# Kernel optimization log

Measured on AMD Instinct MI355X. Metric: run time of the kernel, lower is better.

## Reference

```python
import jax, jax.numpy as jnp
import numpy as np

B, S, D, CH = 2048, 16, 512, 1024


def setup_inputs() -> dict:
    key = jax.random.key(0)
    ks = jax.random.split(key, 12)
    sc = lambda fan: 1.0 / np.sqrt(fan)
    return {
        "local_descs_t": jax.random.normal(ks[0], (B, S, D), jnp.float32),
        "local_descs_rot": jax.random.normal(ks[1], (B, S, D), jnp.float32),
        "w_scene": jax.random.normal(ks[2], (2 * D,), jnp.float32) * sc(2 * D),
        "b_scene": jnp.zeros((1,), jnp.float32),
        "Wh_t": jax.random.normal(ks[3], (S, D, CH), jnp.float32) * sc(D),
        "bh_t": jnp.zeros((S, CH), jnp.float32),
        "Wo_t": jax.random.normal(ks[4], (S, CH, 3), jnp.float32) * sc(CH),
        "bo_t": jnp.zeros((S, 3), jnp.float32),
        "Wh_r": jax.random.normal(ks[5], (S, D, CH), jnp.float32) * sc(D),
        "bh_r": jnp.zeros((S, CH), jnp.float32),
        "Wo_r": jax.random.normal(ks[6], (S, CH, 4), jnp.float32) * sc(CH),
        "bo_r": jnp.zeros((S, 4), jnp.float32),
    }


def _expert_head(x, onehot, Wh, bh, Wo, bo):
    # x: [B, D] gathered global descriptor; run all S experts, combine by one-hot
    h = jax.nn.gelu(jnp.einsum("bd,sdh->bsh", x, Wh) + bh, approximate=False)
    o = jnp.einsum("bsh,sho->bso", h, Wo) + bo  # [B, S, out]
    return jnp.einsum("bs,bso->bo", onehot, o)


def reference(local_descs_t, local_descs_rot, w_scene, b_scene,
              Wh_t, bh_t, Wo_t, bo_t, Wh_r, bh_r, Wo_r, bo_r):
    # scene router: Linear(2D -> 1) over concatenated descriptors, log_softmax over scenes
    cat = jnp.concatenate([local_descs_t, local_descs_rot], axis=2)  # [B, S, 2D]
    logits = jnp.einsum("bsd,d->bs", cat, w_scene) + b_scene[0]
    scene_log_distr = jax.nn.log_softmax(logits, axis=1)  # [B, S]
    max_indices = jnp.argmax(scene_log_distr, axis=1)  # [B]
    onehot = jax.nn.one_hot(max_indices, S, dtype=local_descs_t.dtype)
    # combine: gather selected scene's descriptor (torch code uses dense mask w)
    global_desc_t = jnp.einsum("bs,bsd->bd", onehot, local_descs_t)
    global_desc_rot = jnp.einsum("bs,bsd->bd", onehot, local_descs_rot)
    # per-sample expert heads (Linear -> GELU -> Linear)
    x_t = _expert_head(global_desc_t, onehot, Wh_t, bh_t, Wo_t, bo_t)    # [B, 3]
    x_rot = _expert_head(global_desc_rot, onehot, Wh_r, bh_r, Wo_r, bo_r)  # [B, 4]
    pose = jnp.concatenate([x_t, x_rot], axis=1)  # [B, 7]
    return pose, scene_log_distr
```

## Files before the change

### kernel.cpp

```cpp
#include <hip/hip_runtime.h>
#include <hip/hip_bf16.h>
#include <math.h>

constexpr int B_  = 2048;
constexpr int S_  = 16;
constexpr int D_  = 512;
constexpr int CH_ = 1024;

constexpr int BM = 64;
constexpr int BN = 128;
constexpr int BK = 64;

typedef __attribute__((ext_vector_type(8))) short bf16x8;
typedef __attribute__((ext_vector_type(4))) float f32x4;

constexpr size_t CNT_OFF  = 0;
constexpr size_t LIST_OFF = 256;

static __device__ __forceinline__ short f2bf(float x) {
    __hip_bfloat16 h = __float2bfloat16(x);
    return *(short*)&h;
}

static __device__ __forceinline__ float gelu_exact(float x) {
    return 0.5f * x * (1.f + erff(x * 0.70710678118654752f));
}

__global__ __launch_bounds__(1024) void k_router_sm(
    const float* __restrict__ ldt, const float* __restrict__ ldr,
    const float* __restrict__ w,   const float* __restrict__ bsc,
    float* __restrict__ sld,
    int* __restrict__ count, int* __restrict__ list)
{
    const int b    = blockIdx.x;
    const int wave = threadIdx.x >> 6;
    const int lane = threadIdx.x & 63;

    __shared__ float lgs[S_];

    const float4* pt = (const float4*)(ldt + ((size_t)b * S_ + wave) * D_);
    const float4* pr = (const float4*)(ldr + ((size_t)b * S_ + wave) * D_);
    const float4* wt = (const float4*)(w);
    const float4* wr = (const float4*)(w + D_);

    float acc = 0.f;
    #pragma unroll
    for (int it = 0; it < 2; it++) {
        const int i = lane + it * 64;
        float4 a  = pt[i]; float4 ww = wt[i];
        acc += a.x * ww.x + a.y * ww.y + a.z * ww.z + a.w * ww.w;
        float4 c  = pr[i]; float4 w2 = wr[i];
        acc += c.x * w2.x + c.y * w2.y + c.z * w2.z + c.w * w2.w;
    }
    #pragma unroll
    for (int off = 32; off > 0; off >>= 1) acc += __shfl_down(acc, off, 64);
    if (lane == 0) lgs[wave] = acc;
    __syncthreads();

    if (threadIdx.x < S_) {
        const int s = threadIdx.x;
        const float v = lgs[s] + bsc[0];
        float mv = v; int mi = s;
        #pragma unroll
        for (int d = 1; d < 16; d <<= 1) {
            float ov = __shfl_xor(mv, d, 16);
            int   oi = __shfl_xor(mi, d, 16);
            if (ov > mv || (ov == mv && oi < mi)) { mv = ov; mi = oi; }
        }
        float e = expf(v - mv);
        float sum = e;
        #pragma unroll
        for (int d = 1; d < 16; d <<= 1) sum += __shfl_xor(sum, d, 16);
        const float lse = mv + logf(sum);
        sld[b * S_ + s] = v - lse;
        if (s == 0) {
            const int pos = atomicAdd(&count[mi], 1);
            list[mi * B_ + pos] = b;
        }
    }
}

__global__ __launch_bounds__(256) void k_expert_mfma(
    const float* __restrict__ ldt, const float* __restrict__ ldr,
    const float* __restrict__ Wht, const float* __restrict__ bht,
    const float* __restrict__ Wot, const float* __restrict__ bot,
    const float* __restrict__ Whr, const float* __restrict__ bhr,
    const float* __restrict__ Wor, const float* __restrict__ bor,
    const int* __restrict__ count, const int* __restrict__ list,
    float* __restrict__ pose)
{
    const int bid  = blockIdx.x;
    const int m    = bid & 15;
    const int head = (bid >> 4) & 1;
    const int ct   = (bid >> 5) & 7;
    const int st   = bid >> 8;

    const int n = count[m];
    if (st * BM >= n) return;

    const float* __restrict__ xsrc = head ? ldr : ldt;
    const float* __restrict__ Wh   = head ? Whr : Wht;
    const float* __restrict__ bh   = head ? bhr : bht;
    const float* __restrict__ Wo   = head ? Wor : Wot;
    const float* __restrict__ bo   = head ? bor : bot;
    const int noj    = head ? 4 : 3;
    const int jobase = head ? 3 : 0;

    const int ch0 = ct * BN;

    __shared__ short As[BM * BK];
    __shared__ short Bs[BN * BK];
    __shared__ int   bidx[BM];

    const int tid  = threadIdx.x;
    const int wave = tid >> 6;
    const int lane = tid & 63;
    const int wr   = wave >> 1;
    const int wc   = wave & 1;
    const int rbase = wr * 32;
    const int cbase = wc * 64;

    if (tid < BM) {
        const int gi = st * BM + tid;
        bidx[tid] = (gi < n) ? list[m * B_ + gi] : -1;
    }
    __syncthreads();

    f32x4 acc[2][4] = {};

    for (int k0 = 0; k0 < D_; k0 += BK) {
        {
            const int r  = tid >> 2;
            const int kc = (tid & 3) * 16;
            const int bb = bidx[r];
            float4 v0, v1, v2, v3;
            if (bb >= 0) {
                const float4* src = (const float4*)(xsrc + ((size_t)bb * S_ + m) * D_ + k0 + kc);
                v0 = src[0]; v1 = src[1]; v2 = src[2]; v3 = src[3];
            } else {
                v0 = v1 = v2 = v3 = make_float4(0.f, 0.f, 0.f, 0.f);
            }
            short tmp[16];
            tmp[0]=f2bf(v0.x); tmp[1]=f2bf(v0.y); tmp[2]=f2bf(v0.z); tmp[3]=f2bf(v0.w);
            tmp[4]=f2bf(v1.x); tmp[5]=f2bf(v1.y); tmp[6]=f2bf(v1.z); tmp[7]=f2bf(v1.w);
            tmp[8]=f2bf(v2.x); tmp[9]=f2bf(v2.y); tmp[10]=f2bf(v2.z); tmp[11]=f2bf(v2.w);
            tmp[12]=f2bf(v3.x); tmp[13]=f2bf(v3.y); tmp[14]=f2bf(v3.z); tmp[15]=f2bf(v3.w);
            const int u0 = kc >> 3;
            *(bf16x8*)&As[r * 64 + ((u0     ^ (r & 7)) << 3)] = *(bf16x8*)&tmp[0];
            *(bf16x8*)&As[r * 64 + (((u0+1) ^ (r & 7)) << 3)] = *(bf16x8*)&tmp[8];
        }
        {
            const int k  = tid >> 2;
            const size_t rowbase = (size_t)m * D_ * CH_ + (size_t)(k0 + k) * CH_ + ch0;
            #pragma unroll
            for (int i = 0; i < 8; i++) {
                const int chl = (tid & 3) * 4 + i * 16;
                const float4 wv = *(const float4*)(Wh + rowbase + chl);
                #pragma unroll
                for (int c = 0; c < 4; c++) {
                    const int ch = chl + c;
                    const float f = (c == 0) ? wv.x : (c == 1) ? wv.y : (c == 2) ? wv.z : wv.w;
                    Bs[ch * 64 + (((k >> 3) ^ (ch & 7)) << 3) + (k & 7)] = f2bf(f);
                }
            }
        }
        __syncthreads();

        #pragma unroll
        for (int kk = 0; kk < BK; kk += 32) {
            const int ub = (kk >> 3) + (lane >> 4);
            bf16x8 a[2], bfr[4];
            #pragma unroll
            for (int fm = 0; fm < 2; fm++) {
                const int r = rbase + fm * 16 + (lane & 15);
                a[fm] = *(bf16x8*)&As[r * 64 + ((ub ^ (r & 7)) << 3)];
            }
            #pragma unroll
            for (int fn = 0; fn < 4; fn++) {
                const int c = cbase + fn * 16 + (lane & 15);
                bfr[fn] = *(bf16x8*)&Bs[c * 64 + ((ub ^ (c & 7)) << 3)];
            }
            #pragma unroll
            for (int fm = 0; fm < 2; fm++)
                #pragma unroll
                for (int fn = 0; fn < 4; fn++)
                    acc[fm][fn] = __builtin_amdgcn_mfma_f32_16x16x32_bf16(a[fm], bfr[fn], acc[fm][fn], 0, 0, 0);
        }
        __syncthreads();
    }

    float g[2][4][4];
    float wo_l[4][4];
    #pragma unroll
    for (int fn = 0; fn < 4; fn++) {
        const int ch = ch0 + cbase + fn * 16 + (lane & 15);
        const float bias = bh[m * CH_ + ch];
        #pragma unroll
        for (int fm = 0; fm < 2; fm++)
            #pragma unroll
            for (int j = 0; j < 4; j++)
                g[fm][fn][j] = gelu_exact(acc[fm][fn][j] + bias);
        #pragma unroll
        for (int jo = 0; jo < 4; jo++)
            wo_l[fn][jo] = (jo < noj) ? Wo[(size_t)(m * CH_ + ch) * noj + jo] : 0.f;
    }

    #pragma unroll
    for (int fm = 0; fm < 2; fm++) {
        #pragma unroll
        for (int j = 0; j < 4; j++) {
            const int lr = rbase + fm * 16 + ((lane >> 4) << 2) + j;
            const int bb = bidx[lr];
            #pragma unroll
            for (int jo = 0; jo < 4; jo++) {
                if (jo >= noj) continue;
                float v = 0.f;
                #pragma unroll
                for (int fn = 0; fn < 4; fn++) v += g[fm][fn][j] * wo_l[fn][jo];
                #pragma unroll
                for (int d = 1; d < 16; d <<= 1) v += __shfl_xor(v, d, 16);
                if ((lane & 15) == 0 && bb >= 0) {
                    if (ct == 0 && wc == 0) v += bo[m * noj + jo];
                    atomicAdd(&pose[(size_t)bb * 7 + jobase + jo], v);
                }
            }
        }
    }
}

extern "C" void kernel_launch(void* const* d_in, const int* in_sizes, int n_in,
                              void* d_out, int out_size, void* d_ws, size_t ws_size,
                              hipStream_t stream)
{
    const float* ldt = (const float*)d_in[0];
    const float* ldr = (const float*)d_in[1];
    const float* wsc = (const float*)d_in[2];
    const float* bsc = (const float*)d_in[3];
    const float* Wht = (const float*)d_in[4];
    const float* bht = (const float*)d_in[5];
    const float* Wot = (const float*)d_in[6];
    const float* bot = (const float*)d_in[7];
    const float* Whr = (const float*)d_in[8];
    const float* bhr = (const float*)d_in[9];
    const float* Wor = (const float*)d_in[10];
    const float* bor = (const float*)d_in[11];

    float* pose = (float*)d_out;
    float* sld  = (float*)d_out + (size_t)B_ * 7;

    int* count = (int*)((char*)d_ws + CNT_OFF);
    int* list  = (int*)((char*)d_ws + LIST_OFF);

    hipMemsetAsync(count, 0, 16 * sizeof(int), stream);
    hipMemsetAsync(pose, 0, (size_t)B_ * 7 * sizeof(float), stream);

    k_router_sm<<<dim3(B_), dim3(1024), 0, stream>>>(ldt, ldr, wsc, bsc, sld, count, list);

    k_expert_mfma<<<dim3(16 * 2 * 8 * 32), dim3(256), 0, stream>>>(
        ldt, ldr, Wht, bht, Wot, bot, Whr, bhr, Wor, bor, count, list, pose);
}
```

Measured before the change: 83.11 us.

## Software-pipeline expert GEMM with register prefetch and reshaped tiles

Tiles of the expert GEMM change from BN=128,BK=64 to BN=64,BK=128, with padded LDS strides in place of the XOR swizzle. The K loop is fully unrolled with double-buffered register prefetch, so the global loads for the next tile are in flight during the MFMA work on the current one. The block index order is changed so blocks that share an expert's weights and channel tile run close together. The weight load now reads column-strided scalars, which may hurt coalescing, and the grid doubles, which adds more atomic adds per output.

Result: slower. 107.3 us (+29.1%).

```diff
diff --git a/kernel.cpp b/kernel.cpp
--- a/kernel.cpp
+++ b/kernel.cpp
@@ -8,8 +8,10 @@
 constexpr int CH_ = 1024;
 
 constexpr int BM = 64;
-constexpr int BN = 128;
-constexpr int BK = 64;
+constexpr int BN = 64;
+constexpr int BK = 128;
+constexpr int SA = 136;
+constexpr int SB = 136;
 
 typedef __attribute__((ext_vector_type(8))) short bf16x8;
 typedef __attribute__((ext_vector_type(4))) float f32x4;
@@ -21,7 +23,6 @@
     __hip_bfloat16 h = __float2bfloat16(x);
     return *(short*)&h;
 }
-
 static __device__ __forceinline__ float gelu_exact(float x) {
     return 0.5f * x * (1.f + erff(x * 0.70710678118654752f));
 }
@@ -29,8 +30,7 @@
 __global__ __launch_bounds__(1024) void k_router_sm(
     const float* __restrict__ ldt, const float* __restrict__ ldr,
     const float* __restrict__ w,   const float* __restrict__ bsc,
-    float* __restrict__ sld,
-    int* __restrict__ count, int* __restrict__ list)
+    float* __restrict__ sld, int* __restrict__ count, int* __restrict__ list)
 {
     const int b    = blockIdx.x;
     const int wave = threadIdx.x >> 6;
@@ -67,8 +67,7 @@
             int   oi = __shfl_xor(mi, d, 16);
             if (ov > mv || (ov == mv && oi < mi)) { mv = ov; mi = oi; }
         }
-        float e = expf(v - mv);
-        float sum = e;
+        float sum = expf(v - mv);
         #pragma unroll
         for (int d = 1; d < 16; d <<= 1) sum += __shfl_xor(sum, d, 16);
         const float lse = mv + logf(sum);
@@ -90,10 +89,10 @@
     float* __restrict__ pose)
 {
     const int bid  = blockIdx.x;
-    const int m    = bid & 15;
-    const int head = (bid >> 4) & 1;
-    const int ct   = (bid >> 5) & 7;
-    const int st   = bid >> 8;
+    const int ct   = bid & 15;
+    const int st   = (bid >> 4) & 31;
+    const int head = (bid >> 9) & 1;
+    const int m    = bid >> 10;
 
     const int n = count[m];
     if (st * BM >= n) return;
@@ -105,11 +104,10 @@
     const float* __restrict__ bo   = head ? bor : bot;
     const int noj    = head ? 4 : 3;
     const int jobase = head ? 3 : 0;
-
-    const int ch0 = ct * BN;
-
-    __shared__ short As[BM * BK];
-    __shared__ short Bs[BN * BK];
+    const int ch0    = ct * BN;
+
+    __shared__ short As[BM * SA];
+    __shared__ short Bs[BN * SB];
     __shared__ int   bidx[BM];
 
     const int tid  = threadIdx.x;
@@ -118,7 +116,7 @@
     const int wr   = wave >> 1;
     const int wc   = wave & 1;
     const int rbase = wr * 32;
-    const int cbase = wc * 64;
+    const int cbase = wc * 32;
 
     if (tid < BM) {
         const int gi = st * BM + tid;
@@ -126,73 +124,97 @@
     }
     __syncthreads();
 
-    f32x4 acc[2][4] = {};
-
-    for (int k0 = 0; k0 < D_; k0 += BK) {
-        {
-            const int r  = tid >> 2;
-            const int kc = (tid & 3) * 16;
-            const int bb = bidx[r];
-            float4 v0, v1, v2, v3;
-            if (bb >= 0) {
-                const float4* src = (const float4*)(xsrc + ((size_t)bb * S_ + m) * D_ + k0 + kc);
-                v0 = src[0]; v1 = src[1]; v2 = src[2]; v3 = src[3];
-            } else {
-                v0 = v1 = v2 = v3 = make_float4(0.f, 0.f, 0.f, 0.f);
-            }
-            short tmp[16];
+    const int rA = tid >> 2;
+    const int kq = tid & 3;
+    const int bb = bidx[rA];
+    const float* xrow = (bb >= 0) ? (xsrc + ((size_t)bb * S_ + m) * D_) : nullptr;
+
+    const int u2  = tid >> 5;
+    const int chb = tid & 31;
+    const float* wcol = Wh + (size_t)m * D_ * CH_ + ch0 + chb;
+
+    auto loadA = [&](float4* pa, int t) {
+        if (bb >= 0) {
+            const float4* p = (const float4*)(xrow + t * BK) + kq * 8;
+            #pragma unroll
+            for (int i = 0; i < 8; i++) pa[i] = p[i];
+        } else {
+            #pragma unroll
+            for (int i = 0; i < 8; i++) pa[i] = make_float4(0.f, 0.f, 0.f, 0.f);
+        }
+    };
+    auto loadB = [&](float* pb, int t) {
+        #pragma unroll
+        for (int i = 0; i < 4; i++) {
+            const int uu = u2 * 2 + (i >> 1);
+            const float* p = wcol + (size_t)(t * BK + uu * 8) * CH_ + (i & 1) * 32;
+            #pragma unroll
+            for (int j = 0; j < 8; j++) pb[i * 8 + j] = p[(size_t)j * CH_];
+        }
+    };
+    auto storeTiles = [&](const float4* pa, const float* pb) {
+        #pragma unroll
+        for (int c = 0; c < 4; c++) {
+            short tmp[8];
+            const float4 v0 = pa[c * 2], v1 = pa[c * 2 + 1];
             tmp[0]=f2bf(v0.x); tmp[1]=f2bf(v0.y); tmp[2]=f2bf(v0.z); tmp[3]=f2bf(v0.w);
             tmp[4]=f2bf(v1.x); tmp[5]=f2bf(v1.y); tmp[6]=f2bf(v1.z); tmp[7]=f2bf(v1.w);
-            tmp[8]=f2bf(v2.x); tmp[9]=f2bf(v2.y); tmp[10]=f2bf(v2.z); tmp[11]=f2bf(v2.w);
-            tmp[12]=f2bf(v3.x); tmp[13]=f2bf(v3.y); tmp[14]=f2bf(v3.z); tmp[15]=f2bf(v3.w);
-            const int u0 = kc >> 3;
-            *(bf16x8*)&As[r * 64 + ((u0     ^ (r & 7)) << 3)] = *(bf16x8*)&tmp[0];
-            *(bf16x8*)&As[r * 64 + (((u0+1) ^ (r & 7)) << 3)] = *(bf16x8*)&tmp[8];
-        }
-        {
-            const int k  = tid >> 2;
-            const size_t rowbase = (size_t)m * D_ * CH_ + (size_t)(k0 + k) * CH_ + ch0;
-            #pragma unroll
-            for (int i = 0; i < 8; i++) {
-                const int chl = (tid & 3) * 4 + i * 16;
-                const float4 wv = *(const float4*)(Wh + rowbase + chl);
-                #pragma unroll
-                for (int c = 0; c < 4; c++) {
-                    const int ch = chl + c;
-                    const float f = (c == 0) ? wv.x : (c == 1) ? wv.y : (c == 2) ? wv.z : wv.w;
-                    Bs[ch * 64 + (((k >> 3) ^ (ch & 7)) << 3) + (k & 7)] = f2bf(f);
-                }
-            }
-        }
-        __syncthreads();
-
-        #pragma unroll
-        for (int kk = 0; kk < BK; kk += 32) {
-            const int ub = (kk >> 3) + (lane >> 4);
-            bf16x8 a[2], bfr[4];
-            #pragma unroll
-            for (int fm = 0; fm < 2; fm++) {
-                const int r = rbase + fm * 16 + (lane & 15);
-                a[fm] = *(bf16x8*)&As[r * 64 + ((ub ^ (r & 7)) << 3)];
-            }
-            #pragma unroll
-            for (int fn = 0; fn < 4; fn++) {
-                const int c = cbase + fn * 16 + (lane & 15);
-                bfr[fn] = *(bf16x8*)&Bs[c * 64 + ((ub ^ (c & 7)) << 3)];
-            }
+            *(bf16x8*)&As[rA * SA + kq * 32 + c * 8] = *(bf16x8*)tmp;
+        }
+        #pragma unroll
+        for (int i = 0; i < 4; i++) {
+            const int uu = u2 * 2 + (i >> 1);
+            const int ch = chb + (i & 1) * 32;
+            short tmp[8];
+            #pragma unroll
+            for (int j = 0; j < 8; j++) tmp[j] = f2bf(pb[i * 8 + j]);
+            *(bf16x8*)&Bs[ch * SB + uu * 8] = *(bf16x8*)tmp;
+        }
+    };
+
+    f32x4 acc[2][2] = {};
+    auto mfmaTile = [&]() {
+        #pragma unroll
+        for (int kk = 0; kk < 4; kk++) {
+            const int ub = kk * 4 + (lane >> 4);
+            bf16x8 af[2], bfv[2];
+            #pragma unroll
+            for (int fm = 0; fm < 2; fm++)
+                af[fm] = *(bf16x8*)&As[(rbase + fm * 16 + (lane & 15)) * SA + ub * 8];
+            #pragma unroll
+            for (int fn = 0; fn < 2; fn++)
+                bfv[fn] = *(bf16x8*)&Bs[(cbase + fn * 16 + (lane & 15)) * SB + ub * 8];
             #pragma unroll
             for (int fm = 0; fm < 2; fm++)
                 #pragma unroll
-                for (int fn = 0; fn < 4; fn++)
-                    acc[fm][fn] = __builtin_amdgcn_mfma_f32_16x16x32_bf16(a[fm], bfr[fn], acc[fm][fn], 0, 0, 0);
-        }
-        __syncthreads();
-    }
-
-    float g[2][4][4];
-    float wo_l[4][4];
-    #pragma unroll
-    for (int fn = 0; fn < 4; fn++) {
+                for (int fn = 0; fn < 2; fn++)
+                    acc[fm][fn] = __builtin_amdgcn_mfma_f32_16x16x32_bf16(af[fm], bfv[fn], acc[fm][fn], 0, 0, 0);
+        }
+    };
+
+    float4 pa[8], qa[8];
+    float  pb[32], qb[32];
+    loadA(pa, 0); loadB(pb, 0);
+
+    storeTiles(pa, pb); __syncthreads();
+    loadA(qa, 1); loadB(qb, 1);
+    mfmaTile(); __syncthreads();
+
+    storeTiles(qa, qb); __syncthreads();
+    loadA(pa, 2); loadB(pb, 2);
+    mfmaTile(); __syncthreads();
+
+    storeTiles(pa, pb); __syncthreads();
+    loadA(qa, 3); loadB(qb, 3);
+    mfmaTile(); __syncthreads();
+
+    storeTiles(qa, qb); __syncthreads();
+    mfmaTile(); __syncthreads();
+
+    float g[2][2][4];
+    float wo_l[2][4];
+    #pragma unroll
+    for (int fn = 0; fn < 2; fn++) {
         const int ch = ch0 + cbase + fn * 16 + (lane & 15);
         const float bias = bh[m * CH_ + ch];
         #pragma unroll
@@ -210,18 +232,16 @@
         #pragma unroll
         for (int j = 0; j < 4; j++) {
             const int lr = rbase + fm * 16 + ((lane >> 4) << 2) + j;
-            const int bb = bidx[lr];
+            const int bb2 = bidx[lr];
             #pragma unroll
             for (int jo = 0; jo < 4; jo++) {
                 if (jo >= noj) continue;
-                float v = 0.f;
-                #pragma unroll
-                for (int fn = 0; fn < 4; fn++) v += g[fm][fn][j] * wo_l[fn][jo];
+                float v = g[fm][0][j] * wo_l[0][jo] + g[fm][1][j] * wo_l[1][jo];
                 #pragma unroll
                 for (int d = 1; d < 16; d <<= 1) v += __shfl_xor(v, d, 16);
-                if ((lane & 15) == 0 && bb >= 0) {
+                if ((lane & 15) == 0 && bb2 >= 0) {
                     if (ct == 0 && wc == 0) v += bo[m * noj + jo];
-                    atomicAdd(&pose[(size_t)bb * 7 + jobase + jo], v);
+                    atomicAdd(&pose[(size_t)bb2 * 7 + jobase + jo], v);
                 }
             }
         }
@@ -256,6 +276,6 @@
 
     k_router_sm<<<dim3(B_), dim3(1024), 0, stream>>>(ldt, ldr, wsc, bsc, sld, count, list);
 
-    k_expert_mfma<<<dim3(16 * 2 * 8 * 32), dim3(256), 0, stream>>>(
+    k_expert_mfma<<<dim3(16 * 2 * 32 * 16), dim3(256), 0, stream>>>(
         ldt, ldr, Wht, bht, Wot, bot, Whr, bhr, Wor, bor, count, list, pose);
 }
```

## Pre-gather bf16 descriptors in router and use compact tile list without LDS

Applied to the files above, without the earlier changes.

The router kernel now writes the selected scene's descriptors as bf16 into workspace, so the expert kernel no longer gathers and converts fp32 rows itself. A tiny kernel builds a compact list of (expert, row-tile) pairs, which removes the many blocks that previously launched only to exit early. The expert GEMM drops shared-memory staging: each lane loads A fragments directly and converts strided fp32 weight columns from global memory, using smaller 64-column tiles. This trades LDS reuse and coalesced weight loads for fewer syncs and less wasted launch, at the risk of scattered, uncoalesced weight reads. It also caps the grid at 48 tiles, which relies on the at most 47 tiles 2048 rows over 16 experts can produce.

Result: slower. 130.8 us (+57.4%).

```diff
diff --git a/kernel.cpp b/kernel.cpp
--- a/kernel.cpp
+++ b/kernel.cpp
@@ -7,21 +7,20 @@
 constexpr int D_  = 512;
 constexpr int CH_ = 1024;
 
-constexpr int BM = 64;
-constexpr int BN = 128;
-constexpr int BK = 64;
-
 typedef __attribute__((ext_vector_type(8))) short bf16x8;
 typedef __attribute__((ext_vector_type(4))) float f32x4;
 
 constexpr size_t CNT_OFF  = 0;
-constexpr size_t LIST_OFF = 256;
+constexpr size_t NT_OFF   = 64;
+constexpr size_t TL_OFF   = 128;
+constexpr size_t LIST_OFF = 512;
+constexpr size_t XGT_OFF  = LIST_OFF + (size_t)16 * 2048 * 4;
+constexpr size_t XGR_OFF  = XGT_OFF + (size_t)B_ * D_ * 2;
 
 static __device__ __forceinline__ short f2bf(float x) {
     __hip_bfloat16 h = __float2bfloat16(x);
     return *(short*)&h;
 }
-
 static __device__ __forceinline__ float gelu_exact(float x) {
     return 0.5f * x * (1.f + erff(x * 0.70710678118654752f));
 }
@@ -29,14 +28,15 @@
 __global__ __launch_bounds__(1024) void k_router_sm(
     const float* __restrict__ ldt, const float* __restrict__ ldr,
     const float* __restrict__ w,   const float* __restrict__ bsc,
-    float* __restrict__ sld,
-    int* __restrict__ count, int* __restrict__ list)
+    float* __restrict__ sld, int* __restrict__ count, int* __restrict__ list,
+    unsigned short* __restrict__ xgt, unsigned short* __restrict__ xgr)
 {
     const int b    = blockIdx.x;
     const int wave = threadIdx.x >> 6;
     const int lane = threadIdx.x & 63;
 
     __shared__ float lgs[S_];
+    __shared__ int   smi;
 
     const float4* pt = (const float4*)(ldt + ((size_t)b * S_ + wave) * D_);
     const float4* pr = (const float4*)(ldr + ((size_t)b * S_ + wave) * D_);
@@ -67,133 +67,115 @@
             int   oi = __shfl_xor(mi, d, 16);
             if (ov > mv || (ov == mv && oi < mi)) { mv = ov; mi = oi; }
         }
-        float e = expf(v - mv);
-        float sum = e;
+        float sum = expf(v - mv);
         #pragma unroll
         for (int d = 1; d < 16; d <<= 1) sum += __shfl_xor(sum, d, 16);
         const float lse = mv + logf(sum);
         sld[b * S_ + s] = v - lse;
         if (s == 0) {
+            smi = mi;
             const int pos = atomicAdd(&count[mi], 1);
             list[mi * B_ + pos] = b;
         }
     }
-}
-
-__global__ __launch_bounds__(256) void k_expert_mfma(
-    const float* __restrict__ ldt, const float* __restrict__ ldr,
+    __syncthreads();
+
+    const int mi = smi;
+    const int t = threadIdx.x;
+    if (t < D_) {
+        xgt[(size_t)b * D_ + t] = (unsigned short)f2bf(ldt[((size_t)b * S_ + mi) * D_ + t]);
+    } else {
+        const int t2 = t - D_;
+        xgr[(size_t)b * D_ + t2] = (unsigned short)f2bf(ldr[((size_t)b * S_ + mi) * D_ + t2]);
+    }
+}
+
+__global__ void k_tiles(const int* __restrict__ count, int* __restrict__ ntile,
+                        int* __restrict__ tlist)
+{
+    if (threadIdx.x == 0 && blockIdx.x == 0) {
+        int nt = 0;
+        for (int m = 0; m < S_; m++) {
+            const int c = count[m];
+            const int nst = (c + 63) >> 6;
+            for (int s2 = 0; s2 < nst; s2++) tlist[nt++] = m | (s2 << 8);
+        }
+        ntile[0] = nt;
+    }
+}
+
+__global__ __launch_bounds__(256) void k_expert(
     const float* __restrict__ Wht, const float* __restrict__ bht,
     const float* __restrict__ Wot, const float* __restrict__ bot,
     const float* __restrict__ Whr, const float* __restrict__ bhr,
     const float* __restrict__ Wor, const float* __restrict__ bor,
+    const unsigned short* __restrict__ xgt, const unsigned short* __restrict__ xgr,
     const int* __restrict__ count, const int* __restrict__ list,
+    const int* __restrict__ ntile, const int* __restrict__ tlist,
     float* __restrict__ pose)
 {
     const int bid  = blockIdx.x;
-    const int m    = bid & 15;
+    const int ct   = bid & 15;
     const int head = (bid >> 4) & 1;
-    const int ct   = (bid >> 5) & 7;
-    const int st   = bid >> 8;
-
-    const int n = count[m];
-    if (st * BM >= n) return;
-
-    const float* __restrict__ xsrc = head ? ldr : ldt;
-    const float* __restrict__ Wh   = head ? Whr : Wht;
-    const float* __restrict__ bh   = head ? bhr : bht;
-    const float* __restrict__ Wo   = head ? Wor : Wot;
-    const float* __restrict__ bo   = head ? bor : bot;
+    const int t    = bid >> 5;
+    if (t >= ntile[0]) return;
+    const int tv = tlist[t];
+    const int m  = tv & 255;
+    const int st = tv >> 8;
+    const int n  = count[m];
+
+    const unsigned short* __restrict__ xg = head ? xgr : xgt;
+    const float* __restrict__ Wh = head ? Whr : Wht;
+    const float* __restrict__ bh = head ? bhr : bht;
+    const float* __restrict__ Wo = head ? Wor : Wot;
+    const float* __restrict__ bo = head ? bor : bot;
     const int noj    = head ? 4 : 3;
     const int jobase = head ? 3 : 0;
-
-    const int ch0 = ct * BN;
-
-    __shared__ short As[BM * BK];
-    __shared__ short Bs[BN * BK];
-    __shared__ int   bidx[BM];
 
     const int tid  = threadIdx.x;
     const int wave = tid >> 6;
     const int lane = tid & 63;
-    const int wr   = wave >> 1;
-    const int wc   = wave & 1;
-    const int rbase = wr * 32;
-    const int cbase = wc * 64;
-
-    if (tid < BM) {
-        const int gi = st * BM + tid;
-        bidx[tid] = (gi < n) ? list[m * B_ + gi] : -1;
-    }
-    __syncthreads();
-
-    f32x4 acc[2][4] = {};
-
-    for (int k0 = 0; k0 < D_; k0 += BK) {
-        {
-            const int r  = tid >> 2;
-            const int kc = (tid & 3) * 16;
-            const int bb = bidx[r];
-            float4 v0, v1, v2, v3;
-            if (bb >= 0) {
-                const float4* src = (const float4*)(xsrc + ((size_t)bb * S_ + m) * D_ + k0 + kc);
-                v0 = src[0]; v1 = src[1]; v2 = src[2]; v3 = src[3];
-            } else {
-                v0 = v1 = v2 = v3 = make_float4(0.f, 0.f, 0.f, 0.f);
-            }
-            short tmp[16];
-            tmp[0]=f2bf(v0.x); tmp[1]=f2bf(v0.y); tmp[2]=f2bf(v0.z); tmp[3]=f2bf(v0.w);
-            tmp[4]=f2bf(v1.x); tmp[5]=f2bf(v1.y); tmp[6]=f2bf(v1.z); tmp[7]=f2bf(v1.w);
-            tmp[8]=f2bf(v2.x); tmp[9]=f2bf(v2.y); tmp[10]=f2bf(v2.z); tmp[11]=f2bf(v2.w);
-            tmp[12]=f2bf(v3.x); tmp[13]=f2bf(v3.y); tmp[14]=f2bf(v3.z); tmp[15]=f2bf(v3.w);
-            const int u0 = kc >> 3;
-            *(bf16x8*)&As[r * 64 + ((u0     ^ (r & 7)) << 3)] = *(bf16x8*)&tmp[0];
-            *(bf16x8*)&As[r * 64 + (((u0+1) ^ (r & 7)) << 3)] = *(bf16x8*)&tmp[8];
-        }
-        {
-            const int k  = tid >> 2;
-            const size_t rowbase = (size_t)m * D_ * CH_ + (size_t)(k0 + k) * CH_ + ch0;
-            #pragma unroll
-            for (int i = 0; i < 8; i++) {
-                const int chl = (tid & 3) * 4 + i * 16;
-                const float4 wv = *(const float4*)(Wh + rowbase + chl);
-                #pragma unroll
-                for (int c = 0; c < 4; c++) {
-                    const int ch = chl + c;
-                    const float f = (c == 0) ? wv.x : (c == 1) ? wv.y : (c == 2) ? wv.z : wv.w;
-                    Bs[ch * 64 + (((k >> 3) ^ (ch & 7)) << 3) + (k & 7)] = f2bf(f);
-                }
-            }
-        }
-        __syncthreads();
-
-        #pragma unroll
-        for (int kk = 0; kk < BK; kk += 32) {
-            const int ub = (kk >> 3) + (lane >> 4);
-            bf16x8 a[2], bfr[4];
-            #pragma unroll
-            for (int fm = 0; fm < 2; fm++) {
-                const int r = rbase + fm * 16 + (lane & 15);
-                a[fm] = *(bf16x8*)&As[r * 64 + ((ub ^ (r & 7)) << 3)];
-            }
-            #pragma unroll
-            for (int fn = 0; fn < 4; fn++) {
-                const int c = cbase + fn * 16 + (lane & 15);
-                bfr[fn] = *(bf16x8*)&Bs[c * 64 + ((ub ^ (c & 7)) << 3)];
-            }
-            #pragma unroll
-            for (int fm = 0; fm < 2; fm++)
-                #pragma unroll
-                for (int fn = 0; fn < 4; fn++)
-                    acc[fm][fn] = __builtin_amdgcn_mfma_f32_16x16x32_bf16(a[fm], bfr[fn], acc[fm][fn], 0, 0, 0);
-        }
-        __syncthreads();
-    }
-
-    float g[2][4][4];
-    float wo_l[4][4];
-    #pragma unroll
-    for (int fn = 0; fn < 4; fn++) {
-        const int ch = ch0 + cbase + fn * 16 + (lane & 15);
+    const int wr = wave >> 1, wc = wave & 1;
+    const int l15 = lane & 15, lq = lane >> 4;
+    const int rbase = st * 64 + wr * 32;
+    const int cb    = ct * 64 + wc * 32;
+
+    const unsigned short* arow[2];
+    #pragma unroll
+    for (int fm = 0; fm < 2; fm++) {
+        const int gi = rbase + fm * 16 + l15;
+        const int bb = (gi < n) ? list[m * B_ + gi] : 0;
+        arow[fm] = xg + (size_t)bb * D_ + lq * 8;
+    }
+    const float* wcol = Wh + (size_t)m * D_ * CH_ + (size_t)(lq * 8) * CH_ + cb + l15;
+
+    f32x4 acc[2][2] = {};
+    #pragma unroll 4
+    for (int kk = 0; kk < D_; kk += 32) {
+        bf16x8 a[2];
+        a[0] = *(const bf16x8*)(arow[0] + kk);
+        a[1] = *(const bf16x8*)(arow[1] + kk);
+        bf16x8 bv[2];
+        #pragma unroll
+        for (int fn = 0; fn < 2; fn++) {
+            const float* p = wcol + (size_t)kk * CH_ + fn * 16;
+            short tmp[8];
+            #pragma unroll
+            for (int j = 0; j < 8; j++) tmp[j] = f2bf(p[(size_t)j * CH_]);
+            bv[fn] = *(bf16x8*)tmp;
+        }
+        #pragma unroll
+        for (int fm = 0; fm < 2; fm++)
+            #pragma unroll
+            for (int fn = 0; fn < 2; fn++)
+                acc[fm][fn] = __builtin_amdgcn_mfma_f32_16x16x32_bf16(a[fm], bv[fn], acc[fm][fn], 0, 0, 0);
+    }
+
+    float g[2][2][4];
+    float wo_l[2][4];
+    #pragma unroll
+    for (int fn = 0; fn < 2; fn++) {
+        const int ch = cb + fn * 16 + l15;
         const float bias = bh[m * CH_ + ch];
         #pragma unroll
         for (int fm = 0; fm < 2; fm++)
@@ -209,19 +191,19 @@
     for (int fm = 0; fm < 2; fm++) {
         #pragma unroll
         for (int j = 0; j < 4; j++) {
-            const int lr = rbase + fm * 16 + ((lane >> 4) << 2) + j;
-            const int bb = bidx[lr];
             #pragma unroll
             for (int jo = 0; jo < 4; jo++) {
                 if (jo >= noj) continue;
-                float v = 0.f;
-                #pragma unroll
-                for (int fn = 0; fn < 4; fn++) v += g[fm][fn][j] * wo_l[fn][jo];
+                float v = g[fm][0][j] * wo_l[0][jo] + g[fm][1][j] * wo_l[1][jo];
                 #pragma unroll
                 for (int d = 1; d < 16; d <<= 1) v += __shfl_xor(v, d, 16);
-                if ((lane & 15) == 0 && bb >= 0) {
-                    if (ct == 0 && wc == 0) v += bo[m * noj + jo];
-                    atomicAdd(&pose[(size_t)bb * 7 + jobase + jo], v);
+                if (l15 == 0) {
+                    const int gi = rbase + fm * 16 + lq * 4 + j;
+                    if (gi < n) {
+                        const int bb = list[m * B_ + gi];
+                        if (ct == 0 && wc == 0) v += bo[m * noj + jo];
+                        atomicAdd(&pose[(size_t)bb * 7 + jobase + jo], v);
+                    }
                 }
             }
         }
@@ -249,13 +231,21 @@
     float* sld  = (float*)d_out + (size_t)B_ * 7;
 
     int* count = (int*)((char*)d_ws + CNT_OFF);
+    int* ntile = (int*)((char*)d_ws + NT_OFF);
+    int* tlist = (int*)((char*)d_ws + TL_OFF);
     int* list  = (int*)((char*)d_ws + LIST_OFF);
+    unsigned short* xgt = (unsigned short*)((char*)d_ws + XGT_OFF);
+    unsigned short* xgr = (unsigned short*)((char*)d_ws + XGR_OFF);
 
     hipMemsetAsync(count, 0, 16 * sizeof(int), stream);
     hipMemsetAsync(pose, 0, (size_t)B_ * 7 * sizeof(float), stream);
 
-    k_router_sm<<<dim3(B_), dim3(1024), 0, stream>>>(ldt, ldr, wsc, bsc, sld, count, list);
-
-    k_expert_mfma<<<dim3(16 * 2 * 8 * 32), dim3(256), 0, stream>>>(
-        ldt, ldr, Wht, bht, Wot, bot, Whr, bhr, Wor, bor, count, list, pose);
-}
+    k_router_sm<<<dim3(B_), dim3(1024), 0, stream>>>(
+        ldt, ldr, wsc, bsc, sld, count, list, xgt, xgr);
+
+    k_tiles<<<dim3(1), dim3(64), 0, stream>>>(count, ntile, tlist);
+
+    k_expert<<<dim3(48 * 2 * 16), dim3(256), 0, stream>>>(
+        Wht, bht, Wot, bot, Whr, bhr, Wor, bor,
+        xgt, xgr, count, list, ntile, tlist, pose);
+}
```
